# Kernel tuning notes

Measured on AMD Instinct MI355X. Metric: run time of the kernel, lower is better.

## Reference

```python
import jax, jax.numpy as jnp
import numpy as np

D_MODEL = 2048
D_HID = D_MODEL // 2
NUM_EXPERTS = 16
TOP_K = 2
EPS = 1e-8


def setup_inputs() -> dict:
    key = jax.random.key(0)
    k1, k2, k3, k4, k5 = jax.random.split(key, 5)
    hidden_states = jax.random.normal(k1, (8, 4096, D_MODEL), dtype=jnp.float32)
    # Linear layers: PyTorch stores weight as [out, in]; we keep [in, out] for x @ W.
    s1 = 1.0 / np.sqrt(D_MODEL)
    s2 = 1.0 / np.sqrt(D_HID)
    W1 = jax.random.uniform(k2, (D_MODEL, D_HID), jnp.float32, -s1, s1)
    b1 = jax.random.uniform(k3, (D_HID,), jnp.float32, -s1, s1)
    W2 = jax.random.uniform(k4, (D_HID, NUM_EXPERTS), jnp.float32, -s2, s2)
    b2 = jax.random.uniform(k5, (NUM_EXPERTS,), jnp.float32, -s2, s2)
    return {"hidden_states": hidden_states, "W1": W1, "b1": b1, "W2": W2, "b2": b2}


def reference(hidden_states, W1, b1, W2, b2):
    # 2-layer MLP router (dropout in eval mode -> identity)
    h = jax.nn.relu(jnp.einsum("bsd,dh->bsh", hidden_states, W1) + b1)
    logits = jnp.einsum("bsh,he->bse", h, W2) + b2  # [B, S, E]
    router_probs = jax.nn.softmax(logits, axis=-1)
    top_k_gates, top_k_indices = jax.lax.top_k(router_probs, TOP_K)
    top_k_gates = top_k_gates / (jnp.sum(top_k_gates, axis=-1, keepdims=True) + EPS)
    return top_k_gates, top_k_indices, router_probs
```

## Files before the change

### kernel.cpp

```cpp
#include <hip/hip_runtime.h>
#include <math.h>
#include <stdint.h>

#define TOKENS 32768
#define DM 2048
#define DH 1024
#define NE 16
#define BM 128
#define BN 512
#define NPASS 2
#define BK 16
#define NSTAGE 128
#define RT_TAU 5e-5f
#define FB_TAU 5e-4f
#define XSC 16.0f
#define WSC 64.0f
#define DESC (1.0f/1024.0f)

#define OFF_IDX  (TOKENS * 2)
#define OFF_PROB (TOKENS * 4)

#define WS_LIST 1024
#define WS_WT   132096
#define WIMG_BYTES ((size_t)NSTAGE * NPASS * 32768)
#define WS_NEEDED ((size_t)WS_WT + WIMG_BYTES)
#define RCAP 512

typedef _Float16 f16x8 __attribute__((ext_vector_type(8)));
typedef _Float16 f16x4 __attribute__((ext_vector_type(4)));
typedef short    bf16x8 __attribute__((ext_vector_type(8)));
typedef float    f32x16 __attribute__((ext_vector_type(16)));

static __device__ __forceinline__ void gload_lds16(const void* g, void* l) {
    __builtin_amdgcn_global_load_lds(
        (const __attribute__((address_space(1))) void*)g,
        (__attribute__((address_space(3))) void*)l, 16, 0, 0);
}

__global__ __launch_bounds__(256)
void prep_w16(const float* __restrict__ W1, char* __restrict__ wimg) {
    const int bid = blockIdx.x;
    const int s = bid >> 1, p = bid & 1;
    char* img = wimg + ((size_t)bid << 15);
    const int tid = threadIdx.x;
    #pragma unroll
    for (int rep = 0; rep < 2; ++rep) {
        const int n = tid + rep * 256;
        float w[16];
        #pragma unroll
        for (int j = 0; j < 16; ++j)
            w[j] = W1[(size_t)(s * 16 + j) * DH + p * 512 + n] * WSC;
        #pragma unroll
        for (int q = 0; q < 2; ++q) {
            f16x8 hi, lo;
            #pragma unroll
            for (int j = 0; j < 8; ++j) {
                float ww = w[q * 8 + j];
                _Float16 h = (_Float16)ww;
                hi[j] = h;
                lo[j] = (_Float16)(ww - (float)h);
            }
            *(f16x8*)(img + ((q * 2 + 0) * 512 + n) * 16) = hi;
            *(f16x8*)(img + ((q * 2 + 1) * 512 + n) * 16) = lo;
        }
    }
}

__global__ __launch_bounds__(512, 2)
void router16(const float* __restrict__ x, const char* __restrict__ wimg,
              const float* __restrict__ b1, const float* __restrict__ W2,
              const float* __restrict__ b2, float* __restrict__ out,
              int* __restrict__ cnt, int* __restrict__ list)
{
    __shared__ __align__(16) char xsmem[2][8192];
    __shared__ __align__(16) char bsmem[2][32768];
    __shared__ float w2t[NE * 128];
    __shared__ float ls[BM * 17];

    float* h_lds = (float*)&bsmem[0][0];
    float* lsred = (float*)&bsmem[0][0];

    const int tid  = threadIdx.x;
    const int wid  = tid >> 6;
    const int lane = tid & 63;
    const int l31  = lane & 31;
    const int lh   = lane >> 5;
    const int wm   = wid >> 2;
    const int wn   = wid & 3;
    const int m0   = blockIdx.x * BM;

    const int tq  = tid & 31;
    const int egq = (tid >> 5) & 3;
    const int ns  = tid >> 7;

    const int arow = tid >> 2, kq = tid & 3;
    const int q4 = kq >> 1, half = kq & 1;

    float lacc[4][4];
    #pragma unroll
    for (int i = 0; i < 4; ++i)
        #pragma unroll
        for (int e = 0; e < 4; ++e) lacc[i][e] = 0.f;

    for (int p = 0; p < NPASS; ++p) {
        f32x16 acc[2][4];
        #pragma unroll
        for (int mf = 0; mf < 2; ++mf)
            #pragma unroll
            for (int nf = 0; nf < 4; ++nf)
                #pragma unroll
                for (int q = 0; q < 16; ++q) acc[mf][nf][q] = 0.f;

        {
            const char* img = wimg + ((size_t)(0 * 2 + p) << 15);
            #pragma unroll
            for (int i = 0; i < 4; ++i) {
                int seg = (wid << 2) + i;
                gload_lds16(img + (seg << 10) + (lane << 4), &bsmem[0][seg << 10]);
            }
            const float* xp = x + (size_t)(m0 + arow) * DM + kq * 4;
            float4 v = *(const float4*)xp;
            float f[4] = {v.x * XSC, v.y * XSC, v.z * XSC, v.w * XSC};
            f16x4 hi, lo;
            #pragma unroll
            for (int j = 0; j < 4; ++j) {
                _Float16 h = (_Float16)f[j];
                hi[j] = h;
                lo[j] = (_Float16)(f[j] - (float)h);
            }
            *(f16x4*)(&xsmem[0][((q4 * 2 + 0) * 128 + arow) * 16 + half * 8]) = hi;
            *(f16x4*)(&xsmem[0][((q4 * 2 + 1) * 128 + arow) * 16 + half * 8]) = lo;
        }
        __syncthreads();

        for (int s = 0; s < NSTAGE; ++s) {
            const int cur = s & 1;
            float4 xr;
            if (s < NSTAGE - 1) {
                const char* img = wimg + ((size_t)((s + 1) * 2 + p) << 15);
                #pragma unroll
                for (int i = 0; i < 4; ++i) {
                    int seg = (wid << 2) + i;
                    gload_lds16(img + (seg << 10) + (lane << 4), &bsmem[cur ^ 1][seg << 10]);
                }
                xr = *(const float4*)(x + (size_t)(m0 + arow) * DM + (s + 1) * BK + kq * 4);
            }
            {
                const int q = lh;
                const char* xb = &xsmem[cur][0];
                const char* bb = &bsmem[cur][0];
                f16x8 ah[2], al[2], bh[4], bl[4];
                #pragma unroll
                for (int mf = 0; mf < 2; ++mf) {
                    int m = wm * 64 + mf * 32 + l31;
                    ah[mf] = *(const f16x8*)(xb + ((q * 2 + 0) * 128 + m) * 16);
                    al[mf] = *(const f16x8*)(xb + ((q * 2 + 1) * 128 + m) * 16);
                }
                #pragma unroll
                for (int nf = 0; nf < 4; ++nf) {
                    int n = wn * 128 + nf * 32 + l31;
                    bh[nf] = *(const f16x8*)(bb + ((q * 2 + 0) * 512 + n) * 16);
                    bl[nf] = *(const f16x8*)(bb + ((q * 2 + 1) * 512 + n) * 16);
                }
                #pragma unroll
                for (int mf = 0; mf < 2; ++mf)
                    #pragma unroll
                    for (int nf = 0; nf < 4; ++nf) {
                        acc[mf][nf] = __builtin_amdgcn_mfma_f32_32x32x16_f16(ah[mf], bh[nf], acc[mf][nf], 0, 0, 0);
                        acc[mf][nf] = __builtin_amdgcn_mfma_f32_32x32x16_f16(ah[mf], bl[nf], acc[mf][nf], 0, 0, 0);
                        acc[mf][nf] = __builtin_amdgcn_mfma_f32_32x32x16_f16(al[mf], bh[nf], acc[mf][nf], 0, 0, 0);
                    }
            }
            if (s < NSTAGE - 1) {
                float f[4] = {xr.x * XSC, xr.y * XSC, xr.z * XSC, xr.w * XSC};
                f16x4 hi, lo;
                #pragma unroll
                for (int j = 0; j < 4; ++j) {
                    _Float16 h = (_Float16)f[j];
                    hi[j] = h;
                    lo[j] = (_Float16)(f[j] - (float)h);
                }
                *(f16x4*)(&xsmem[cur ^ 1][((q4 * 2 + 0) * 128 + arow) * 16 + half * 8]) = hi;
                *(f16x4*)(&xsmem[cur ^ 1][((q4 * 2 + 1) * 128 + arow) * 16 + half * 8]) = lo;
            }
            __syncthreads();
        }

        for (int ch = 0; ch < 4; ++ch) {
            __syncthreads();
            if (wn == ch) {
                #pragma unroll
                for (int nf = 0; nf < 4; ++nf) {
                    int col = nf * 32 + l31;
                    float bb = b1[p * BN + ch * 128 + col];
                    #pragma unroll
                    for (int mf = 0; mf < 2; ++mf)
                        #pragma unroll
                        for (int r = 0; r < 16; ++r) {
                            int row = wm * 64 + mf * 32 + (r & 3) + 8 * (r >> 2) + 4 * lh;
                            h_lds[row * 128 + col] = fmaxf(acc[mf][nf][r] * DESC + bb, 0.f);
                        }
                }
            }
            #pragma unroll
            for (int q = 0; q < 4; ++q) {
                int i = tid * 4 + q;
                int nn = i >> 4, e = i & 15;
                w2t[e * 128 + nn] = W2[(size_t)(p * BN + ch * 128 + nn) * NE + e];
            }
            __syncthreads();
            for (int nn = 0; nn < 32; ++nn) {
                int nL = ns * 32 + ((nn + tq) & 31);
                float hv[4], wv[4];
                #pragma unroll
                for (int i = 0; i < 4; ++i) hv[i] = h_lds[(tq * 4 + i) * 128 + nL];
                #pragma unroll
                for (int e = 0; e < 4; ++e) wv[e] = w2t[(egq * 4 + e) * 128 + nL];
                #pragma unroll
                for (int i = 0; i < 4; ++i)
                    #pragma unroll
                    for (int e = 0; e < 4; ++e)
                        lacc[i][e] = fmaf(hv[i], wv[e], lacc[i][e]);
            }
        }
        __syncthreads();
    }

    __syncthreads();
    #pragma unroll
    for (int i = 0; i < 4; ++i)
        #pragma unroll
        for (int e = 0; e < 4; ++e)
            lsred[((tq * 4 + i) * 16 + egq * 4 + e) * 4 + ns] = lacc[i][e];
    __syncthreads();
    #pragma unroll
    for (int q = 0; q < 4; ++q) {
        int idx = tid * 4 + q;
        int t = idx >> 4, e = idx & 15;
        ls[t * 17 + e] = lsred[idx * 4 + 0] + lsred[idx * 4 + 1] +
                         lsred[idx * 4 + 2] + lsred[idx * 4 + 3] + b2[e];
    }
    __syncthreads();

    if (tid < BM) {
        int t = tid;
        float l[NE]; float mx = -1e30f;
        #pragma unroll
        for (int e = 0; e < NE; ++e) { l[e] = ls[t * 17 + e]; mx = fmaxf(mx, l[e]); }
        float pb[NE]; float ssum = 0.f;
        #pragma unroll
        for (int e = 0; e < NE; ++e) { pb[e] = expf(l[e] - mx); ssum += pb[e]; }
        float inv = 1.f / ssum;
        #pragma unroll
        for (int e = 0; e < NE; ++e) pb[e] *= inv;

        int i1 = 0; float p1 = pb[0];
        #pragma unroll
        for (int e = 1; e < NE; ++e) if (pb[e] > p1) { p1 = pb[e]; i1 = e; }
        int i2 = -1; float p2 = -1.f;
        #pragma unroll
        for (int e = 0; e < NE; ++e) if (e != i1 && pb[e] > p2) { p2 = pb[e]; i2 = e; }
        float p3 = -1.f;
        #pragma unroll
        for (int e = 0; e < NE; ++e) if (e != i1 && e != i2 && pb[e] > p3) p3 = pb[e];

        float denom = p1 + p2 + 1e-8f;
        size_t gt = (size_t)(m0 + t);
        out[gt * 2 + 0] = p1 / denom;
        out[gt * 2 + 1] = p2 / denom;
        out[OFF_IDX + gt * 2 + 0] = (float)i1;
        out[OFF_IDX + gt * 2 + 1] = (float)i2;
        #pragma unroll
        for (int e = 0; e < NE; ++e) out[OFF_PROB + gt * 16 + e] = pb[e];

        if (p1 - p2 < RT_TAU || p2 - p3 < RT_TAU) {
            int k = atomicAdd(cnt, 1);
            list[k] = m0 + t;
        }
    }
}

__global__ __launch_bounds__(256, 4)
void repair_partial(const float* __restrict__ x, const float* __restrict__ W1,
                    const int* __restrict__ cnt, const int* __restrict__ list,
                    float* __restrict__ hpart)
{
    __shared__ float xsl[4][512];
    __shared__ int tokid[4];
    const int tid = threadIdx.x;
    int nrep = cnt[0]; if (nrep > RCAP) nrep = RCAP;
    const int g = blockIdx.x >> 2, ks = blockIdx.x & 3;
    if (g * 4 >= nrep) return;

    if (tid < 4) {
        int j = g * 4 + tid;
        tokid[tid] = list[j < nrep ? j : 0];
    }
    __syncthreads();
    #pragma unroll
    for (int i = 0; i < 2; ++i) {
        int slot = tid + i * 256;
        int t = slot >> 7, c = slot & 127;
        *(float4*)(&xsl[t][c * 4]) =
            *(const float4*)(x + (size_t)tokid[t] * DM + ks * 512 + c * 4);
    }
    __syncthreads();

    float acc[4][4];
    #pragma unroll
    for (int t = 0; t < 4; ++t)
        #pragma unroll
        for (int q = 0; q < 4; ++q) acc[t][q] = 0.f;

    for (int k4 = 0; k4 < 128; ++k4) {
        float4 xv[4];
        #pragma unroll
        for (int t = 0; t < 4; ++t) xv[t] = *(const float4*)(&xsl[t][k4 * 4]);
        #pragma unroll
        for (int kk = 0; kk < 4; ++kk) {
            const float4 w = *(const float4*)(W1 + (size_t)(ks * 512 + k4 * 4 + kk) * DH + tid * 4);
            #pragma unroll
            for (int t = 0; t < 4; ++t) {
                const float a = ((const float*)&xv[t])[kk];
                acc[t][0] = fmaf(a, w.x, acc[t][0]);
                acc[t][1] = fmaf(a, w.y, acc[t][1]);
                acc[t][2] = fmaf(a, w.z, acc[t][2]);
                acc[t][3] = fmaf(a, w.w, acc[t][3]);
            }
        }
    }
    #pragma unroll
    for (int t = 0; t < 4; ++t)
        *(float4*)(hpart + (size_t)(g * 16 + ks * 4 + t) * 1024 + tid * 4) =
            make_float4(acc[t][0], acc[t][1], acc[t][2], acc[t][3]);
}

__global__ __launch_bounds__(256, 2)
void repair_final(const float* __restrict__ hpart, const float* __restrict__ b1,
                  const float* __restrict__ W2, const float* __restrict__ b2,
                  float* __restrict__ out,
                  const int* __restrict__ cnt, const int* __restrict__ list)
{
    __shared__ float hsh[4][DH];
    __shared__ float red[256];
    __shared__ float lg[4][NE];
    __shared__ int tokid[4];
    const int tid = threadIdx.x;
    int nrep = cnt[0]; if (nrep > RCAP) nrep = RCAP;
    const int g = blockIdx.x;
    if (g * 4 >= nrep) return;

    if (tid < 4) {
        int j = g * 4 + tid;
        tokid[tid] = list[j < nrep ? j : 0];
    }
    __syncthreads();
    #pragma unroll
    for (int i = 0; i < 4; ++i) {
        int slot = tid + i * 256;
        int t = slot >> 8, c = slot & 255;
        float4 s0 = *(const float4*)(hpart + (size_t)(g * 16 + 0 * 4 + t) * 1024 + c * 4);
        float4 s1 = *(const float4*)(hpart + (size_t)(g * 16 + 1 * 4 + t) * 1024 + c * 4);
        float4 s2 = *(const float4*)(hpart + (size_t)(g * 16 + 2 * 4 + t) * 1024 + c * 4);
        float4 s3 = *(const float4*)(hpart + (size_t)(g * 16 + 3 * 4 + t) * 1024 + c * 4);
        float4 bv = *(const float4*)(b1 + c * 4);
        float4 h;
        h.x = fmaxf(s0.x + s1.x + s2.x + s3.x + bv.x, 0.f);
        h.y = fmaxf(s0.y + s1.y + s2.y + s3.y + bv.y, 0.f);
        h.z = fmaxf(s0.z + s1.z + s2.z + s3.z + bv.z, 0.f);
        h.w = fmaxf(s0.w + s1.w + s2.w + s3.w + bv.w, 0.f);
        *(float4*)(&hsh[t][c * 4]) = h;
    }
    __syncthreads();
    {
        const int e  = tid & 15;
        const int t  = (tid >> 4) & 3;
        const int sl = tid >> 6;
        float ps = 0.f;
        for (int q = 0; q < 256; ++q) {
            int n = sl * 256 + q;
            ps = fmaf(hsh[t][n], W2[n * NE + e], ps);
        }
        red[tid] = ps;
    }
    __syncthreads();
    if (tid < 64) {
        int t = tid >> 4, e = tid & 15;
        lg[t][e] = b2[e] + red[0 * 64 + t * 16 + e] + red[1 * 64 + t * 16 + e]
                         + red[2 * 64 + t * 16 + e] + red[3 * 64 + t * 16 + e];
    }
    __syncthreads();
    if (tid < 4 && g * 4 + tid < nrep) {
        const int t = tid;
        float l[NE]; float mx = -1e30f;
        #pragma unroll
        for (int e = 0; e < NE; ++e) { l[e] = lg[t][e]; mx = fmaxf(mx, l[e]); }
        float pb[NE]; float ssum = 0.f;
        #pragma unroll
        for (int e = 0; e < NE; ++e) { pb[e] = expf(l[e] - mx); ssum += pb[e]; }
        float inv = 1.f / ssum;
        #pragma unroll
        for (int e = 0; e < NE; ++e) pb[e] *= inv;
        int i1 = 0; float p1 = pb[0];
        #pragma unroll
        for (int e = 1; e < NE; ++e) if (pb[e] > p1) { p1 = pb[e]; i1 = e; }
        int i2 = -1; float p2 = -1.f;
        #pragma unroll
        for (int e = 0; e < NE; ++e) if (e != i1 && pb[e] > p2) { p2 = pb[e]; i2 = e; }
        float denom = p1 + p2 + 1e-8f;
        size_t gt = (size_t)tokid[t];
        out[gt * 2 + 0] = p1 / denom;
        out[gt * 2 + 1] = p2 / denom;
        out[OFF_IDX + gt * 2 + 0] = (float)i1;
        out[OFF_IDX + gt * 2 + 1] = (float)i2;
        #pragma unroll
        for (int e = 0; e < NE; ++e) out[OFF_PROB + gt * 16 + e] = pb[e];
    }
}

__global__ __launch_bounds__(256, 3)
void repair4(const float* __restrict__ x, const float* __restrict__ W1,
             const float* __restrict__ b1, const float* __restrict__ W2,
             const float* __restrict__ b2, float* __restrict__ out,
             const int* __restrict__ cnt, const int* __restrict__ list, int g0)
{
    __shared__ float xsh[4][DM];
    __shared__ float hsh[4][DH];
    __shared__ float red[256];
    __shared__ float lg[4][NE];
    __shared__ int   tokid[4];

    const int tid  = threadIdx.x;
    const int nrep = cnt[0];

    for (int g = g0 + blockIdx.x; g * 4 < nrep; g += gridDim.x) {
        __syncthreads();
        if (tid < 4) {
            int j = g * 4 + tid;
            tokid[tid] = list[j < nrep ? j : 0];
        }
        __syncthreads();
        #pragma unroll
        for (int i = 0; i < 8; ++i) {
            int slot = tid + i * 256;
            int t = slot >> 9, c = slot & 511;
            *(float4*)(&xsh[t][c * 4]) =
                *(const float4*)(x + (size_t)tokid[t] * DM + c * 4);
        }
        __syncthreads();

        float acc[4][4];
        #pragma unroll
        for (int t = 0; t < 4; ++t)
            #pragma unroll
            for (int q = 0; q < 4; ++q) acc[t][q] = 0.f;

        for (int k4 = 0; k4 < DM / 4; ++k4) {
            float4 xv[4];
            #pragma unroll
            for (int t = 0; t < 4; ++t) xv[t] = *(const float4*)(&xsh[t][k4 * 4]);
            #pragma unroll
            for (int kk = 0; kk < 4; ++kk) {
                const float4 w = *(const float4*)(W1 + (size_t)(k4 * 4 + kk) * DH + tid * 4);
                #pragma unroll
                for (int t = 0; t < 4; ++t) {
                    const float a = ((const float*)&xv[t])[kk];
                    acc[t][0] = fmaf(a, w.x, acc[t][0]);
                    acc[t][1] = fmaf(a, w.y, acc[t][1]);
                    acc[t][2] = fmaf(a, w.z, acc[t][2]);
                    acc[t][3] = fmaf(a, w.w, acc[t][3]);
                }
            }
        }
        {
            const float4 bv = *(const float4*)(b1 + tid * 4);
            #pragma unroll
            for (int t = 0; t < 4; ++t) {
                float4 h;
                h.x = fmaxf(acc[t][0] + bv.x, 0.f);
                h.y = fmaxf(acc[t][1] + bv.y, 0.f);
                h.z = fmaxf(acc[t][2] + bv.z, 0.f);
                h.w = fmaxf(acc[t][3] + bv.w, 0.f);
                *(float4*)(&hsh[t][tid * 4]) = h;
            }
        }
        __syncthreads();
        {
            const int e  = tid & 15;
            const int t  = (tid >> 4) & 3;
            const int sl = tid >> 6;
            float ps = 0.f;
            for (int q = 0; q < 256; ++q) {
                int n = sl * 256 + q;
                ps = fmaf(hsh[t][n], W2[n * NE + e], ps);
            }
            red[tid] = ps;
        }
        __syncthreads();
        if (tid < 64) {
            int t = tid >> 4, e = tid & 15;
            lg[t][e] = b2[e] + red[0 * 64 + t * 16 + e] + red[1 * 64 + t * 16 + e]
                             + red[2 * 64 + t * 16 + e] + red[3 * 64 + t * 16 + e];
        }
        __syncthreads();
        if (tid < 4 && g * 4 + tid < nrep) {
            const int t = tid;
            float l[NE]; float mx = -1e30f;
            #pragma unroll
            for (int e = 0; e < NE; ++e) { l[e] = lg[t][e]; mx = fmaxf(mx, l[e]); }
            float pb[NE]; float ssum = 0.f;
            #pragma unroll
            for (int e = 0; e < NE; ++e) { pb[e] = expf(l[e] - mx); ssum += pb[e]; }
            float inv = 1.f / ssum;
            #pragma unroll
            for (int e = 0; e < NE; ++e) pb[e] *= inv;
            int i1 = 0; float p1 = pb[0];
            #pragma unroll
            for (int e = 1; e < NE; ++e) if (pb[e] > p1) { p1 = pb[e]; i1 = e; }
            int i2 = -1; float p2 = -1.f;
            #pragma unroll
            for (int e = 0; e < NE; ++e) if (e != i1 && pb[e] > p2) { p2 = pb[e]; i2 = e; }
            float denom = p1 + p2 + 1e-8f;
            size_t gt = (size_t)tokid[t];
            out[gt * 2 + 0] = p1 / denom;
            out[gt * 2 + 1] = p2 / denom;
            out[OFF_IDX + gt * 2 + 0] = (float)i1;
            out[OFF_IDX + gt * 2 + 1] = (float)i2;
            #pragma unroll
            for (int e = 0; e < NE; ++e) out[OFF_PROB + gt * 16 + e] = pb[e];
        }
    }
}

__global__ __launch_bounds__(512, 2)
void router_fb(const float* __restrict__ x, const float* __restrict__ W1,
               const float* __restrict__ b1, const float* __restrict__ W2,
               const float* __restrict__ b2, float* __restrict__ out,
               int* __restrict__ cnt, int* __restrict__ list)
{
    __shared__ short xs[BM * 64];
    __shared__ short bs[BN * 64];
    __shared__ float w2t[NE * 128];
    __shared__ float ls[BM * 17];

    float* h_lds = (float*)bs;
    float* lsred = (float*)bs;

    const int tid  = threadIdx.x;
    const int wid  = tid >> 6;
    const int lane = tid & 63;
    const int l31  = lane & 31;
    const int lh   = lane >> 5;
    const int sg   = lane & 7;
    const int wm   = wid >> 2;
    const int wn   = wid & 3;
    const int m0   = blockIdx.x * BM;

    const int tq  = tid & 31;
    const int egq = (tid >> 5) & 3;
    const int ns  = tid >> 7;

    float lacc[4][4];
    #pragma unroll
    for (int i = 0; i < 4; ++i)
        #pragma unroll
        for (int e = 0; e < 4; ++e) lacc[i][e] = 0.f;

    const int arow = tid >> 2, kq = tid & 3;
    const int asig = arow & 7;
    const int nloc = (wid << 6) + lane;
    const int sgl  = lane & 7;

    for (int p = 0; p < NPASS; ++p) {
        f32x16 acc[2][4];
        #pragma unroll
        for (int mf = 0; mf < 2; ++mf)
            #pragma unroll
            for (int nf = 0; nf < 4; ++nf)
                #pragma unroll
                for (int q = 0; q < 16; ++q) acc[mf][nf][q] = 0.f;

        for (int s = 0; s < 64; ++s) {
            __syncthreads();
            {
                const float* wp = W1 + (size_t)(s * 32) * DH + p * BN + nloc;
                short* rb = bs + nloc * 64;
                #pragma unroll
                for (int h = 0; h < 2; ++h) {
                    float f[16];
                    #pragma unroll
                    for (int j = 0; j < 16; ++j)
                        f[j] = wp[(size_t)(h * 16 + j) * DH];
                    uint32_t hd[8], ld_[8];
                    #pragma unroll
                    for (int q = 0; q < 8; ++q) {
                        uint32_t u0 = __float_as_uint(f[2 * q]);
                        uint32_t u1 = __float_as_uint(f[2 * q + 1]);
                        hd[q] = (u0 >> 16) | (u1 & 0xFFFF0000u);
                        float r0 = f[2 * q]     - __uint_as_float(u0 & 0xFFFF0000u);
                        float r1 = f[2 * q + 1] - __uint_as_float(u1 & 0xFFFF0000u);
                        ld_[q] = (__float_as_uint(r0) >> 16) | (__float_as_uint(r1) & 0xFFFF0000u);
                    }
                    *(int4*)(rb + (((2 * h + 0) ^ sgl) << 3)) = make_int4(hd[0], hd[1], hd[2], hd[3]);
                    *(int4*)(rb + (((2 * h + 1) ^ sgl) << 3)) = make_int4(hd[4], hd[5], hd[6], hd[7]);
                    *(int4*)(rb + (((4 + 2 * h + 0) ^ sgl) << 3)) = make_int4(ld_[0], ld_[1], ld_[2], ld_[3]);
                    *(int4*)(rb + (((4 + 2 * h + 1) ^ sgl) << 3)) = make_int4(ld_[4], ld_[5], ld_[6], ld_[7]);
                }
            }
            {
                const float* xp = x + (size_t)(m0 + arow) * DM + s * 32 + kq * 8;
                float4 v0 = *(const float4*)xp;
                float4 v1 = *(const float4*)(xp + 4);
                float f[8] = {v0.x, v0.y, v0.z, v0.w, v1.x, v1.y, v1.z, v1.w};
                uint32_t hd[4], ld_[4];
                #pragma unroll
                for (int q = 0; q < 4; ++q) {
                    uint32_t u0 = __float_as_uint(f[2 * q]);
                    uint32_t u1 = __float_as_uint(f[2 * q + 1]);
                    hd[q] = (u0 >> 16) | (u1 & 0xFFFF0000u);
                    float r0 = f[2 * q]     - __uint_as_float(u0 & 0xFFFF0000u);
                    float r1 = f[2 * q + 1] - __uint_as_float(u1 & 0xFFFF0000u);
                    ld_[q] = (__float_as_uint(r0) >> 16) | (__float_as_uint(r1) & 0xFFFF0000u);
                }
                short* ra = xs + arow * 64;
                *(int4*)(ra + ((kq ^ asig) << 3))       = make_int4(hd[0], hd[1], hd[2], hd[3]);
                *(int4*)(ra + (((4 + kq) ^ asig) << 3)) = make_int4(ld_[0], ld_[1], ld_[2], ld_[3]);
            }
            __syncthreads();
            #pragma unroll
            for (int ks = 0; ks < 2; ++ks) {
                bf16x8 a0[2], a1[2], b0[4], b1f[4];
                #pragma unroll
                for (int mf = 0; mf < 2; ++mf) {
                    int base = (wm * 64 + mf * 32 + l31) * 64;
                    a0[mf] = *(const bf16x8*)(xs + base + (((ks * 2 + lh)) ^ sg) * 8);
                    a1[mf] = *(const bf16x8*)(xs + base + (((4 + ks * 2 + lh)) ^ sg) * 8);
                }
                #pragma unroll
                for (int nf = 0; nf < 4; ++nf) {
                    int base = (wn * 128 + nf * 32 + l31) * 64;
                    b0[nf]  = *(const bf16x8*)(bs + base + (((ks * 2 + lh)) ^ sg) * 8);
                    b1f[nf] = *(const bf16x8*)(bs + base + (((4 + ks * 2 + lh)) ^ sg) * 8);
                }
                #pragma unroll
                for (int mf = 0; mf < 2; ++mf)
                    #pragma unroll
                    for (int nf = 0; nf < 4; ++nf) {
                        acc[mf][nf] = __builtin_amdgcn_mfma_f32_32x32x16_bf16(a0[mf], b0[nf],  acc[mf][nf], 0, 0, 0);
                        acc[mf][nf] = __builtin_amdgcn_mfma_f32_32x32x16_bf16(a0[mf], b1f[nf], acc[mf][nf], 0, 0, 0);
                        acc[mf][nf] = __builtin_amdgcn_mfma_f32_32x32x16_bf16(a1[mf], b0[nf],  acc[mf][nf], 0, 0, 0);
                    }
            }
        }

        for (int ch = 0; ch < 4; ++ch) {
            __syncthreads();
            if (wn == ch) {
                #pragma unroll
                for (int nf = 0; nf < 4; ++nf) {
                    int col = nf * 32 + l31;
                    float bb = b1[p * BN + ch * 128 + col];
                    #pragma unroll
                    for (int mf = 0; mf < 2; ++mf)
                        #pragma unroll
                        for (int r = 0; r < 16; ++r) {
                            int row = wm * 64 + mf * 32 + (r & 3) + 8 * (r >> 2) + 4 * lh;
                            h_lds[row * 128 + col] = fmaxf(acc[mf][nf][r] + bb, 0.f);
                        }
                }
            }
            #pragma unroll
            for (int q = 0; q < 4; ++q) {
                int i = tid * 4 + q;
                int nn = i >> 4, e = i & 15;
                w2t[e * 128 + nn] = W2[(size_t)(p * BN + ch * 128 + nn) * NE + e];
            }
            __syncthreads();
            for (int nn = 0; nn < 32; ++nn) {
                int nL = ns * 32 + ((nn + tq) & 31);
                float hv[4], wv[4];
                #pragma unroll
                for (int i = 0; i < 4; ++i) hv[i] = h_lds[(tq * 4 + i) * 128 + nL];
                #pragma unroll
                for (int e = 0; e < 4; ++e) wv[e] = w2t[(egq * 4 + e) * 128 + nL];
                #pragma unroll
                for (int i = 0; i < 4; ++i)
                    #pragma unroll
                    for (int e = 0; e < 4; ++e)
                        lacc[i][e] = fmaf(hv[i], wv[e], lacc[i][e]);
            }
        }
    }

    __syncthreads();
    #pragma unroll
    for (int i = 0; i < 4; ++i)
        #pragma unroll
        for (int e = 0; e < 4; ++e)
            lsred[((tq * 4 + i) * 16 + egq * 4 + e) * 4 + ns] = lacc[i][e];
    __syncthreads();
    #pragma unroll
    for (int q = 0; q < 4; ++q) {
        int idx = tid * 4 + q;
        int t = idx >> 4, e = idx & 15;
        ls[t * 17 + e] = lsred[idx * 4 + 0] + lsred[idx * 4 + 1] +
                         lsred[idx * 4 + 2] + lsred[idx * 4 + 3] + b2[e];
    }
    __syncthreads();

    if (tid < BM) {
        int t = tid;
        float l[NE]; float mx = -1e30f;
        #pragma unroll
        for (int e = 0; e < NE; ++e) { l[e] = ls[t * 17 + e]; mx = fmaxf(mx, l[e]); }
        float pb[NE]; float ssum = 0.f;
        #pragma unroll
        for (int e = 0; e < NE; ++e) { pb[e] = expf(l[e] - mx); ssum += pb[e]; }
        float inv = 1.f / ssum;
        #pragma unroll
        for (int e = 0; e < NE; ++e) pb[e] *= inv;

        int i1 = 0; float p1 = pb[0];
        #pragma unroll
        for (int e = 1; e < NE; ++e) if (pb[e] > p1) { p1 = pb[e]; i1 = e; }
        int i2 = -1; float p2 = -1.f;
        #pragma unroll
        for (int e = 0; e < NE; ++e) if (e != i1 && pb[e] > p2) { p2 = pb[e]; i2 = e; }
        float p3 = -1.f;
        #pragma unroll
        for (int e = 0; e < NE; ++e) if (e != i1 && e != i2 && pb[e] > p3) p3 = pb[e];

        float denom = p1 + p2 + 1e-8f;
        size_t gt = (size_t)(m0 + t);
        out[gt * 2 + 0] = p1 / denom;
        out[gt * 2 + 1] = p2 / denom;
        out[OFF_IDX + gt * 2 + 0] = (float)i1;
        out[OFF_IDX + gt * 2 + 1] = (float)i2;
        #pragma unroll
        for (int e = 0; e < NE; ++e) out[OFF_PROB + gt * 16 + e] = pb[e];

        if (p1 - p2 < FB_TAU || p2 - p3 < FB_TAU) {
            int k = atomicAdd(cnt, 1);
            list[k] = m0 + t;
        }
    }
}

extern "C" void kernel_launch(void* const* d_in, const int* in_sizes, int n_in,
                              void* d_out, int out_size, void* d_ws, size_t ws_size,
                              hipStream_t stream) {
    const float* x  = (const float*)d_in[0];
    const float* W1 = (const float*)d_in[1];
    const float* b1 = (const float*)d_in[2];
    const float* W2 = (const float*)d_in[3];
    const float* b2 = (const float*)d_in[4];
    float* out = (float*)d_out;

    int*   cnt   = (int*)d_ws;
    int*   list  = (int*)((char*)d_ws + WS_LIST);
    char*  wimg  = (char*)d_ws + WS_WT;
    float* hpart = (float*)wimg;

    hipMemsetAsync(cnt, 0, sizeof(int), stream);
    if (ws_size >= WS_NEEDED) {
        hipLaunchKernelGGL(prep_w16, dim3(NSTAGE * NPASS), dim3(256), 0, stream, W1, wimg);
        hipLaunchKernelGGL(router16, dim3(TOKENS / BM), dim3(512), 0, stream,
                           x, wimg, b1, W2, b2, out, cnt, list);
        hipLaunchKernelGGL(repair_partial, dim3(512), dim3(256), 0, stream,
                           x, W1, cnt, list, hpart);
        hipLaunchKernelGGL(repair_final, dim3(128), dim3(256), 0, stream,
                           hpart, b1, W2, b2, out, cnt, list);
        hipLaunchKernelGGL(repair4, dim3(512), dim3(256), 0, stream,
                           x, W1, b1, W2, b2, out, cnt, list, RCAP / 4);
    } else {
        hipLaunchKernelGGL(router_fb, dim3(TOKENS / BM), dim3(512), 0, stream,
                           x, W1, b1, W2, b2, out, cnt, list);
        hipLaunchKernelGGL(repair4, dim3(512), dim3(256), 0, stream,
                           x, W1, b1, W2, b2, out, cnt, list, 0);
    }
}
```

Measured before the change: 517.5 us.

## Load activations directly into registers, drop LDS staging, use manual waitcnt barriers

Each wave now loads its own activation rows straight from global memory into registers and splits them into hi/lo fp16 fragments there, removing the x LDS buffer and its store/load round trip. The stage loop uses explicit vmcnt waits with raw s_barrier instead of __syncthreads, and raises wave priority around the MFMA block. In exchange, each x element is loaded redundantly by the four column waves (wn), register pressure rises, and the hand-written waitcnt counts must match the number of outstanding loads for correctness.

```diff
diff --git a/kernel.cpp b/kernel.cpp
--- a/kernel.cpp
+++ b/kernel.cpp
@@ -31,10 +31,23 @@
 typedef short    bf16x8 __attribute__((ext_vector_type(8)));
 typedef float    f32x16 __attribute__((ext_vector_type(16)));
 
+#define CFENCE asm volatile("" ::: "memory")
+
 static __device__ __forceinline__ void gload_lds16(const void* g, void* l) {
     __builtin_amdgcn_global_load_lds(
         (const __attribute__((address_space(1))) void*)g,
         (__attribute__((address_space(3))) void*)l, 16, 0, 0);
+}
+
+static __device__ __forceinline__ void cvt_split8(float4 u, float4 v, f16x8& hi, f16x8& lo) {
+    float f[8] = {u.x * XSC, u.y * XSC, u.z * XSC, u.w * XSC,
+                  v.x * XSC, v.y * XSC, v.z * XSC, v.w * XSC};
+    #pragma unroll
+    for (int j = 0; j < 8; ++j) {
+        _Float16 h = (_Float16)f[j];
+        hi[j] = h;
+        lo[j] = (_Float16)(f[j] - (float)h);
+    }
 }
 
 __global__ __launch_bounds__(256)
@@ -72,7 +85,6 @@
               const float* __restrict__ b2, float* __restrict__ out,
               int* __restrict__ cnt, int* __restrict__ list)
 {
-    __shared__ __align__(16) char xsmem[2][8192];
     __shared__ __align__(16) char bsmem[2][32768];
     __shared__ float w2t[NE * 128];
     __shared__ float ls[BM * 17];
@@ -93,8 +105,8 @@
     const int egq = (tid >> 5) & 3;
     const int ns  = tid >> 7;
 
-    const int arow = tid >> 2, kq = tid & 3;
-    const int q4 = kq >> 1, half = kq & 1;
+    const float* xrow0 = x + (size_t)(m0 + wm * 64 + 0 * 32 + l31) * DM + lh * 8;
+    const float* xrow1 = x + (size_t)(m0 + wm * 64 + 1 * 32 + l31) * DM + lh * 8;
 
     float lacc[4][4];
     #pragma unroll
@@ -110,6 +122,8 @@
             for (int nf = 0; nf < 4; ++nf)
                 #pragma unroll
                 for (int q = 0; q < 16; ++q) acc[mf][nf][q] = 0.f;
+
+        f16x8 ah[2], al[2];
 
         {
             const char* img = wimg + ((size_t)(0 * 2 + p) << 15);
@@ -118,24 +132,30 @@
                 int seg = (wid << 2) + i;
                 gload_lds16(img + (seg << 10) + (lane << 4), &bsmem[0][seg << 10]);
             }
-            const float* xp = x + (size_t)(m0 + arow) * DM + kq * 4;
-            float4 v = *(const float4*)xp;
-            float f[4] = {v.x * XSC, v.y * XSC, v.z * XSC, v.w * XSC};
-            f16x4 hi, lo;
-            #pragma unroll
-            for (int j = 0; j < 4; ++j) {
-                _Float16 h = (_Float16)f[j];
-                hi[j] = h;
-                lo[j] = (_Float16)(f[j] - (float)h);
-            }
-            *(f16x4*)(&xsmem[0][((q4 * 2 + 0) * 128 + arow) * 16 + half * 8]) = hi;
-            *(f16x4*)(&xsmem[0][((q4 * 2 + 1) * 128 + arow) * 16 + half * 8]) = lo;
-        }
-        __syncthreads();
+            float4 xa0 = *(const float4*)(xrow0);
+            float4 xa1 = *(const float4*)(xrow0 + 4);
+            float4 xb0 = *(const float4*)(xrow1);
+            float4 xb1 = *(const float4*)(xrow1 + 4);
+            cvt_split8(xa0, xa1, ah[0], al[0]);
+            cvt_split8(xb0, xb1, ah[1], al[1]);
+            asm volatile("s_waitcnt vmcnt(0)" ::: "memory");
+            CFENCE; __builtin_amdgcn_s_barrier(); CFENCE;
+        }
 
         for (int s = 0; s < NSTAGE; ++s) {
             const int cur = s & 1;
-            float4 xr;
+            float4 xa0, xa1, xb0, xb1;
+            if (s < NSTAGE - 1) {
+                const int off = (s + 1) * BK;
+                xa0 = *(const float4*)(xrow0 + off);
+                xa1 = *(const float4*)(xrow0 + off + 4);
+                xb0 = *(const float4*)(xrow1 + off);
+                xb1 = *(const float4*)(xrow1 + off + 4);
+            }
+            if (s < NSTAGE - 1) asm volatile("s_waitcnt vmcnt(4)" ::: "memory");
+            else                asm volatile("s_waitcnt vmcnt(0)" ::: "memory");
+            CFENCE; __builtin_amdgcn_s_barrier(); CFENCE;
+            __builtin_amdgcn_sched_barrier(0);
             if (s < NSTAGE - 1) {
                 const char* img = wimg + ((size_t)((s + 1) * 2 + p) << 15);
                 #pragma unroll
@@ -143,25 +163,18 @@
                     int seg = (wid << 2) + i;
                     gload_lds16(img + (seg << 10) + (lane << 4), &bsmem[cur ^ 1][seg << 10]);
                 }
-                xr = *(const float4*)(x + (size_t)(m0 + arow) * DM + (s + 1) * BK + kq * 4);
             }
             {
+                const char* bb = &bsmem[cur][0];
                 const int q = lh;
-                const char* xb = &xsmem[cur][0];
-                const char* bb = &bsmem[cur][0];
-                f16x8 ah[2], al[2], bh[4], bl[4];
-                #pragma unroll
-                for (int mf = 0; mf < 2; ++mf) {
-                    int m = wm * 64 + mf * 32 + l31;
-                    ah[mf] = *(const f16x8*)(xb + ((q * 2 + 0) * 128 + m) * 16);
-                    al[mf] = *(const f16x8*)(xb + ((q * 2 + 1) * 128 + m) * 16);
-                }
+                f16x8 bh[4], bl[4];
                 #pragma unroll
                 for (int nf = 0; nf < 4; ++nf) {
                     int n = wn * 128 + nf * 32 + l31;
                     bh[nf] = *(const f16x8*)(bb + ((q * 2 + 0) * 512 + n) * 16);
                     bl[nf] = *(const f16x8*)(bb + ((q * 2 + 1) * 512 + n) * 16);
                 }
+                __builtin_amdgcn_s_setprio(1);
                 #pragma unroll
                 for (int mf = 0; mf < 2; ++mf)
                     #pragma unroll
@@ -170,21 +183,14 @@
                         acc[mf][nf] = __builtin_amdgcn_mfma_f32_32x32x16_f16(ah[mf], bl[nf], acc[mf][nf], 0, 0, 0);
                         acc[mf][nf] = __builtin_amdgcn_mfma_f32_32x32x16_f16(al[mf], bh[nf], acc[mf][nf], 0, 0, 0);
                     }
+                __builtin_amdgcn_s_setprio(0);
             }
             if (s < NSTAGE - 1) {
-                float f[4] = {xr.x * XSC, xr.y * XSC, xr.z * XSC, xr.w * XSC};
-                f16x4 hi, lo;
-                #pragma unroll
-                for (int j = 0; j < 4; ++j) {
-                    _Float16 h = (_Float16)f[j];
-                    hi[j] = h;
-                    lo[j] = (_Float16)(f[j] - (float)h);
-                }
-                *(f16x4*)(&xsmem[cur ^ 1][((q4 * 2 + 0) * 128 + arow) * 16 + half * 8]) = hi;
-                *(f16x4*)(&xsmem[cur ^ 1][((q4 * 2 + 1) * 128 + arow) * 16 + half * 8]) = lo;
-            }
-            __syncthreads();
-        }
+                cvt_split8(xa0, xa1, ah[0], al[0]);
+                cvt_split8(xb0, xb1, ah[1], al[1]);
+            }
+        }
+        __syncthreads();
 
         for (int ch = 0; ch < 4; ++ch) {
             __syncthreads();
```

Result: slower. 762.7 us (+47.4%).

## Halve router token tile to 64 rows and pack LDS into one buffer

Applied to the files above, without the earlier changes.

Reduces the router kernel's token tile from 128 to 64 rows, so each wave holds one M fragment and the grid doubles to 512 blocks. Shared memory is merged into a single 72KB buffer, and the launch bound is raised to request more resident blocks. The activation-loading and logit-reduction index maps are rewritten for the smaller tile. The goal is more parallelism and better latency hiding, at the cost of twice as many reads of the shared weight image and fewer MFMAs per LDS B-tile load.

```diff
diff --git a/kernel.cpp b/kernel.cpp
--- a/kernel.cpp
+++ b/kernel.cpp
@@ -6,7 +6,7 @@
 #define DM 2048
 #define DH 1024
 #define NE 16
-#define BM 128
+#define BM 64
 #define BN 512
 #define NPASS 2
 #define BK 16
@@ -27,7 +27,7 @@
 #define RCAP 512
 
 typedef _Float16 f16x8 __attribute__((ext_vector_type(8)));
-typedef _Float16 f16x4 __attribute__((ext_vector_type(4)));
+typedef _Float16 f16x2 __attribute__((ext_vector_type(2)));
 typedef short    bf16x8 __attribute__((ext_vector_type(8)));
 typedef float    f32x16 __attribute__((ext_vector_type(16)));
 
@@ -66,19 +66,17 @@
     }
 }
 
-__global__ __launch_bounds__(512, 2)
+__global__ __launch_bounds__(512, 4)
 void router16(const float* __restrict__ x, const char* __restrict__ wimg,
               const float* __restrict__ b1, const float* __restrict__ W2,
               const float* __restrict__ b2, float* __restrict__ out,
               int* __restrict__ cnt, int* __restrict__ list)
 {
-    __shared__ __align__(16) char xsmem[2][8192];
-    __shared__ __align__(16) char bsmem[2][32768];
-    __shared__ float w2t[NE * 128];
-    __shared__ float ls[BM * 17];
-
-    float* h_lds = (float*)&bsmem[0][0];
-    float* lsred = (float*)&bsmem[0][0];
+    __shared__ __align__(16) char smem[73728];
+    float* h_lds = (float*)smem;
+    float* w2t   = (float*)(smem + 32768);
+    float* lsred = (float*)smem;
+    float* ls    = (float*)(smem + 40960);
 
     const int tid  = threadIdx.x;
     const int wid  = tid >> 6;
@@ -89,12 +87,13 @@
     const int wn   = wid & 3;
     const int m0   = blockIdx.x * BM;
 
-    const int tq  = tid & 31;
-    const int egq = (tid >> 5) & 3;
-    const int ns  = tid >> 7;
-
-    const int arow = tid >> 2, kq = tid & 3;
-    const int q4 = kq >> 1, half = kq & 1;
+    const int tq  = tid & 15;
+    const int egq = (tid >> 4) & 3;
+    const int ns  = tid >> 6;
+
+    const int arow = tid >> 3, ke = tid & 7;
+    const int qa = ke >> 2, ja = (ke & 3) * 4;
+    const float* xrow = x + (size_t)(m0 + arow) * DM + ke * 2;
 
     float lacc[4][4];
     #pragma unroll
@@ -103,59 +102,49 @@
         for (int e = 0; e < 4; ++e) lacc[i][e] = 0.f;
 
     for (int p = 0; p < NPASS; ++p) {
-        f32x16 acc[2][4];
-        #pragma unroll
-        for (int mf = 0; mf < 2; ++mf)
-            #pragma unroll
-            for (int nf = 0; nf < 4; ++nf)
-                #pragma unroll
-                for (int q = 0; q < 16; ++q) acc[mf][nf][q] = 0.f;
+        f32x16 acc[4];
+        #pragma unroll
+        for (int nf = 0; nf < 4; ++nf)
+            #pragma unroll
+            for (int q = 0; q < 16; ++q) acc[nf][q] = 0.f;
 
         {
             const char* img = wimg + ((size_t)(0 * 2 + p) << 15);
             #pragma unroll
             for (int i = 0; i < 4; ++i) {
                 int seg = (wid << 2) + i;
-                gload_lds16(img + (seg << 10) + (lane << 4), &bsmem[0][seg << 10]);
-            }
-            const float* xp = x + (size_t)(m0 + arow) * DM + kq * 4;
-            float4 v = *(const float4*)xp;
-            float f[4] = {v.x * XSC, v.y * XSC, v.z * XSC, v.w * XSC};
-            f16x4 hi, lo;
-            #pragma unroll
-            for (int j = 0; j < 4; ++j) {
-                _Float16 h = (_Float16)f[j];
-                hi[j] = h;
-                lo[j] = (_Float16)(f[j] - (float)h);
-            }
-            *(f16x4*)(&xsmem[0][((q4 * 2 + 0) * 128 + arow) * 16 + half * 8]) = hi;
-            *(f16x4*)(&xsmem[0][((q4 * 2 + 1) * 128 + arow) * 16 + half * 8]) = lo;
+                gload_lds16(img + (seg << 10) + (lane << 4), smem + (seg << 10));
+            }
+            float2 v = *(const float2*)(xrow);
+            _Float16 h0 = (_Float16)(v.x * XSC); float r0 = v.x * XSC - (float)h0;
+            _Float16 h1 = (_Float16)(v.y * XSC); float r1 = v.y * XSC - (float)h1;
+            f16x2 hp = {h0, h1}, lp = {(_Float16)r0, (_Float16)r1};
+            char* xb = smem + 65536;
+            *(f16x2*)(xb + ((qa * 2 + 0) * 64 + arow) * 16 + ja) = hp;
+            *(f16x2*)(xb + ((qa * 2 + 1) * 64 + arow) * 16 + ja) = lp;
         }
         __syncthreads();
 
         for (int s = 0; s < NSTAGE; ++s) {
             const int cur = s & 1;
-            float4 xr;
+            float2 xr;
             if (s < NSTAGE - 1) {
                 const char* img = wimg + ((size_t)((s + 1) * 2 + p) << 15);
                 #pragma unroll
                 for (int i = 0; i < 4; ++i) {
                     int seg = (wid << 2) + i;
-                    gload_lds16(img + (seg << 10) + (lane << 4), &bsmem[cur ^ 1][seg << 10]);
-                }
-                xr = *(const float4*)(x + (size_t)(m0 + arow) * DM + (s + 1) * BK + kq * 4);
+                    gload_lds16(img + (seg << 10) + (lane << 4),
+                                smem + ((cur ^ 1) << 15) + (seg << 10));
+                }
+                xr = *(const float2*)(xrow + (s + 1) * BK);
             }
             {
+                const char* bb = smem + (cur << 15);
+                const char* xb = smem + 65536 + (cur << 12);
                 const int q = lh;
-                const char* xb = &xsmem[cur][0];
-                const char* bb = &bsmem[cur][0];
-                f16x8 ah[2], al[2], bh[4], bl[4];
-                #pragma unroll
-                for (int mf = 0; mf < 2; ++mf) {
-                    int m = wm * 64 + mf * 32 + l31;
-                    ah[mf] = *(const f16x8*)(xb + ((q * 2 + 0) * 128 + m) * 16);
-                    al[mf] = *(const f16x8*)(xb + ((q * 2 + 1) * 128 + m) * 16);
-                }
+                f16x8 ah = *(const f16x8*)(xb + ((q * 2 + 0) * 64 + (wm * 32 + l31)) * 16);
+                f16x8 al = *(const f16x8*)(xb + ((q * 2 + 1) * 64 + (wm * 32 + l31)) * 16);
+                f16x8 bh[4], bl[4];
                 #pragma unroll
                 for (int nf = 0; nf < 4; ++nf) {
                     int n = wn * 128 + nf * 32 + l31;
@@ -163,28 +152,23 @@
                     bl[nf] = *(const f16x8*)(bb + ((q * 2 + 1) * 512 + n) * 16);
                 }
                 #pragma unroll
-                for (int mf = 0; mf < 2; ++mf)
-                    #pragma unroll
-                    for (int nf = 0; nf < 4; ++nf) {
-                        acc[mf][nf] = __builtin_amdgcn_mfma_f32_32x32x16_f16(ah[mf], bh[nf], acc[mf][nf], 0, 0, 0);
-                        acc[mf][nf] = __builtin_amdgcn_mfma_f32_32x32x16_f16(ah[mf], bl[nf], acc[mf][nf], 0, 0, 0);
-                        acc[mf][nf] = __builtin_amdgcn_mfma_f32_32x32x16_f16(al[mf], bh[nf], acc[mf][nf], 0, 0, 0);
-                    }
+                for (int nf = 0; nf < 4; ++nf) {
+                    acc[nf] = __builtin_amdgcn_mfma_f32_32x32x16_f16(ah, bh[nf], acc[nf], 0, 0, 0);
+                    acc[nf] = __builtin_amdgcn_mfma_f32_32x32x16_f16(ah, bl[nf], acc[nf], 0, 0, 0);
+                    acc[nf] = __builtin_amdgcn_mfma_f32_32x32x16_f16(al, bh[nf], acc[nf], 0, 0, 0);
+                }
             }
             if (s < NSTAGE - 1) {
-                float f[4] = {xr.x * XSC, xr.y * XSC, xr.z * XSC, xr.w * XSC};
-                f16x4 hi, lo;
-                #pragma unroll
-                for (int j = 0; j < 4; ++j) {
-                    _Float16 h = (_Float16)f[j];
-                    hi[j] = h;
-                    lo[j] = (_Float16)(f[j] - (float)h);
-                }
-                *(f16x4*)(&xsmem[cur ^ 1][((q4 * 2 + 0) * 128 + arow) * 16 + half * 8]) = hi;
-                *(f16x4*)(&xsmem[cur ^ 1][((q4 * 2 + 1) * 128 + arow) * 16 + half * 8]) = lo;
+                _Float16 h0 = (_Float16)(xr.x * XSC); float r0 = xr.x * XSC - (float)h0;
+                _Float16 h1 = (_Float16)(xr.y * XSC); float r1 = xr.y * XSC - (float)h1;
+                f16x2 hp = {h0, h1}, lp = {(_Float16)r0, (_Float16)r1};
+                char* xb = smem + 65536 + ((cur ^ 1) << 12);
+                *(f16x2*)(xb + ((qa * 2 + 0) * 64 + arow) * 16 + ja) = hp;
+                *(f16x2*)(xb + ((qa * 2 + 1) * 64 + arow) * 16 + ja) = lp;
             }
             __syncthreads();
         }
+        __syncthreads();
 
         for (int ch = 0; ch < 4; ++ch) {
             __syncthreads();
@@ -194,12 +178,10 @@
                     int col = nf * 32 + l31;
                     float bb = b1[p * BN + ch * 128 + col];
                     #pragma unroll
-                    for (int mf = 0; mf < 2; ++mf)
-                        #pragma unroll
-                        for (int r = 0; r < 16; ++r) {
-                            int row = wm * 64 + mf * 32 + (r & 3) + 8 * (r >> 2) + 4 * lh;
-                            h_lds[row * 128 + col] = fmaxf(acc[mf][nf][r] * DESC + bb, 0.f);
-                        }
+                    for (int r = 0; r < 16; ++r) {
+                        int row = wm * 32 + (r & 3) + 8 * (r >> 2) + 4 * lh;
+                        h_lds[row * 128 + col] = fmaxf(acc[nf][r] * DESC + bb, 0.f);
+                    }
                 }
             }
             #pragma unroll
@@ -209,8 +191,9 @@
                 w2t[e * 128 + nn] = W2[(size_t)(p * BN + ch * 128 + nn) * NE + e];
             }
             __syncthreads();
-            for (int nn = 0; nn < 32; ++nn) {
-                int nL = ns * 32 + ((nn + tq) & 31);
+            #pragma unroll
+            for (int nn = 0; nn < 16; ++nn) {
+                int nL = ns * 16 + ((nn + tq) & 15);
                 float hv[4], wv[4];
                 #pragma unroll
                 for (int i = 0; i < 4; ++i) hv[i] = h_lds[(tq * 4 + i) * 128 + nL];
@@ -231,14 +214,16 @@
     for (int i = 0; i < 4; ++i)
         #pragma unroll
         for (int e = 0; e < 4; ++e)
-            lsred[((tq * 4 + i) * 16 + egq * 4 + e) * 4 + ns] = lacc[i][e];
-    __syncthreads();
-    #pragma unroll
-    for (int q = 0; q < 4; ++q) {
-        int idx = tid * 4 + q;
+            lsred[((tq * 4 + i) * 16 + egq * 4 + e) * 8 + ns] = lacc[i][e];
+    __syncthreads();
+    #pragma unroll
+    for (int q = 0; q < 2; ++q) {
+        int idx = tid * 2 + q;
         int t = idx >> 4, e = idx & 15;
-        ls[t * 17 + e] = lsred[idx * 4 + 0] + lsred[idx * 4 + 1] +
-                         lsred[idx * 4 + 2] + lsred[idx * 4 + 3] + b2[e];
+        float ssum = 0.f;
+        #pragma unroll
+        for (int sl = 0; sl < 8; ++sl) ssum += lsred[idx * 8 + sl];
+        ls[t * 17 + e] = ssum + b2[e];
     }
     __syncthreads();
 
@@ -538,10 +523,10 @@
                const float* __restrict__ b2, float* __restrict__ out,
                int* __restrict__ cnt, int* __restrict__ list)
 {
-    __shared__ short xs[BM * 64];
+    __shared__ short xs[128 * 64];
     __shared__ short bs[BN * 64];
     __shared__ float w2t[NE * 128];
-    __shared__ float ls[BM * 17];
+    __shared__ float ls[128 * 17];
 
     float* h_lds = (float*)bs;
     float* lsred = (float*)bs;
@@ -554,7 +539,7 @@
     const int sg   = lane & 7;
     const int wm   = wid >> 2;
     const int wn   = wid & 3;
-    const int m0   = blockIdx.x * BM;
+    const int m0   = blockIdx.x * 128;
 
     const int tq  = tid & 31;
     const int egq = (tid >> 5) & 3;
@@ -708,7 +693,7 @@
     }
     __syncthreads();
 
-    if (tid < BM) {
+    if (tid < 128) {
         int t = tid;
         float l[NE]; float mx = -1e30f;
         #pragma unroll
@@ -773,7 +758,7 @@
         hipLaunchKernelGGL(repair4, dim3(512), dim3(256), 0, stream,
                            x, W1, b1, W2, b2, out, cnt, list, RCAP / 4);
     } else {
-        hipLaunchKernelGGL(router_fb, dim3(TOKENS / BM), dim3(512), 0, stream,
+        hipLaunchKernelGGL(router_fb, dim3(TOKENS / 128), dim3(512), 0, stream,
                            x, W1, b1, W2, b2, out, cnt, list);
         hipLaunchKernelGGL(repair4, dim3(512), dim3(256), 0, stream,
                            x, W1, b1, W2, b2, out, cnt, list, 0);
```

Result: slower. 720.8 us (+39.3%).
